# Kernel tuning notes

Measured on AMD Instinct MI355X. Metric: run time of the kernel, lower is better.

Reference implementation:

```python
import jax, jax.numpy as jnp
import numpy as np

NEG_SLOPE = 0.2  # PyG GATConv default negative_slope


def gat_conv(x, edge_index, W, att_src, att_dst, bias):
    """PyG-style GATConv (concat heads, add_self_loops=True, eval mode).
    x: [N, F_in], edge_index: [2, E] (row 0 = src j, row 1 = dst i).
    W: [F_in, H*C], att_src/att_dst: [H, C], bias: [H*C].
    """
    N = x.shape[0]
    H, C = att_src.shape
    loops = jnp.arange(N, dtype=edge_index.dtype)
    src = jnp.concatenate([edge_index[0], loops])  # [E+N]
    dst = jnp.concatenate([edge_index[1], loops])
    h = (x @ W).reshape(N, H, C)                              # [N,H,C]
    a_src = jnp.einsum('nhc,hc->nh', h, att_src)              # [N,H]
    a_dst = jnp.einsum('nhc,hc->nh', h, att_dst)
    alpha = jax.nn.leaky_relu(a_src[src] + a_dst[dst], NEG_SLOPE)  # [E+N,H]
    # segment softmax over edges sharing the same destination node
    m = jax.ops.segment_max(alpha, dst, num_segments=N)       # [N,H]
    e = jnp.exp(alpha - jax.lax.stop_gradient(m)[dst])
    denom = jax.ops.segment_sum(e, dst, num_segments=N)       # [N,H]
    a = e / (denom[dst] + 1e-16)                              # [E+N,H]
    msg = h[src] * a[:, :, None]                              # [E+N,H,C]
    out = jax.ops.segment_sum(msg, dst, num_segments=N)       # [N,H,C]
    return out.reshape(N, H * C) + bias


def setup_inputs() -> dict:
    key = jax.random.key(0)
    ks = jax.random.split(key, 10)
    N, F, NC, C1, H1 = 50000, 128, 40, 16, 8
    E = 800000
    x = jax.random.normal(ks[0], (N, F), dtype=jnp.float32)
    edge_index = jax.random.randint(ks[1], (2, E), 0, N, dtype=jnp.int64)
    s1 = 1.0 / np.sqrt(F)
    W1 = jax.random.uniform(ks[2], (F, H1 * C1), jnp.float32, -s1, s1)
    att_src1 = jax.random.uniform(ks[3], (H1, C1), jnp.float32, -1.0, 1.0) * s1
    att_dst1 = jax.random.uniform(ks[4], (H1, C1), jnp.float32, -1.0, 1.0) * s1
    bias1 = jnp.zeros((H1 * C1,), jnp.float32)
    s2 = 1.0 / np.sqrt(H1 * C1)
    W2 = jax.random.uniform(ks[5], (H1 * C1, NC), jnp.float32, -s2, s2)
    att_src2 = jax.random.uniform(ks[6], (1, NC), jnp.float32, -1.0, 1.0) * s2
    att_dst2 = jax.random.uniform(ks[7], (1, NC), jnp.float32, -1.0, 1.0) * s2
    bias2 = jnp.zeros((NC,), jnp.float32)
    return {"x": x, "edge_index": edge_index, "W1": W1, "att_src1": att_src1,
            "att_dst1": att_dst1, "bias1": bias1, "W2": W2, "att_src2": att_src2,
            "att_dst2": att_dst2, "bias2": bias2}


def reference(x, edge_index, W1, att_src1, att_dst1, bias1, W2, att_src2, att_dst2, bias2):
    h = gat_conv(x, edge_index, W1, att_src1, att_dst1, bias1)   # [N, 128]
    # dropout in eval mode = identity
    out = gat_conv(h, edge_index, W2, att_src2, att_dst2, bias2)  # [N, 40]
    return out
```

## Files before the change

### kernel.cpp

```cpp
#include <hip/hip_runtime.h>
#include <hip/hip_bf16.h>
#include <math.h>

#define NEG_SLOPE 0.2f

__device__ __forceinline__ float lrelu(float x) { return x > 0.f ? x : NEG_SLOPE * x; }

__device__ __forceinline__ unsigned int pack_bf2(float a, float b) {
    unsigned int ua = __float_as_uint(a);
    ua = (ua + 0x7fffu + ((ua >> 16) & 1u)) >> 16;
    unsigned int ub = __float_as_uint(b);
    ub = (ub + 0x7fffu + ((ub >> 16) & 1u)) & 0xffff0000u;
    return ua | ub;
}
__device__ __forceinline__ float bf_lo(unsigned int u) { return __uint_as_float(u << 16); }
__device__ __forceinline__ float bf_hi(unsigned int u) { return __uint_as_float(u & 0xffff0000u); }

__global__ __launch_bounds__(256) void k_hist(const int* __restrict__ ei, int E, int N,
                                              int* __restrict__ cnt, int* __restrict__ rank) {
    int e = blockIdx.x * 256 + threadIdx.x;
    if (e >= E + N) return;
    int d = (e < E) ? ei[E + e] : (e - E);
    rank[e] = atomicAdd(&cnt[d], 1);
}

__global__ __launch_bounds__(256) void k_scan_part(const int* __restrict__ cnt, int N,
                                                   int* __restrict__ psum) {
    __shared__ int sh[256];
    int t = threadIdx.x;
    int base = blockIdx.x * 1024 + t * 4;
    int tl = 0;
#pragma unroll
    for (int j = 0; j < 4; ++j) tl += (base + j < N) ? cnt[base + j] : 0;
    sh[t] = tl; __syncthreads();
    for (int off = 128; off > 0; off >>= 1) {
        if (t < off) sh[t] += sh[t + off];
        __syncthreads();
    }
    if (t == 0) psum[blockIdx.x] = sh[0];
}

__global__ __launch_bounds__(256) void k_scan_mid(int* __restrict__ psum, int nb) {
    __shared__ int sh[256];
    int t = threadIdx.x;
    int v = (t < nb) ? psum[t] : 0;
    sh[t] = v; __syncthreads();
    for (int off = 1; off < 256; off <<= 1) {
        int a = (t >= off) ? sh[t - off] : 0;
        __syncthreads();
        sh[t] += a;
        __syncthreads();
    }
    psum[t] = sh[t] - v;
}

__global__ __launch_bounds__(256) void k_scan_add(const int* __restrict__ cnt, int N,
                                                  const int* __restrict__ psum,
                                                  int* __restrict__ rowptr) {
    __shared__ int sh[256];
    int t = threadIdx.x;
    int base = blockIdx.x * 1024 + t * 4;
    int c[4]; int tl = 0;
#pragma unroll
    for (int j = 0; j < 4; ++j) { c[j] = (base + j < N) ? cnt[base + j] : 0; tl += c[j]; }
    sh[t] = tl; __syncthreads();
    for (int off = 1; off < 256; off <<= 1) {
        int a = (t >= off) ? sh[t - off] : 0;
        __syncthreads();
        sh[t] += a;
        __syncthreads();
    }
    int run = psum[blockIdx.x] + (sh[t] - tl);
#pragma unroll
    for (int j = 0; j < 4; ++j) {
        if (base + j < N) { rowptr[base + j] = run; run += c[j]; }
    }
}

__global__ __launch_bounds__(256) void k_scatter(const int* __restrict__ ei, int E, int N,
                                                 const int* __restrict__ rowptr,
                                                 const int* __restrict__ rank,
                                                 int* __restrict__ col) {
    int e = blockIdx.x * 256 + threadIdx.x;
    if (e >= E + N) return;
    int s, d;
    if (e < E) { s = ei[e]; d = ei[E + e]; } else { s = d = e - E; }
    col[rowptr[d] + rank[e]] = s;
}

__global__ __launch_bounds__(256) void k_gemm1(const float* __restrict__ x,
                                               const float* __restrict__ W,
                                               const float* __restrict__ att_s,
                                               const float* __restrict__ att_d,
                                               unsigned int* __restrict__ h1A,
                                               unsigned int* __restrict__ h1B,
                                               float* __restrict__ a_src,
                                               float* __restrict__ a_dst, int N) {
    __shared__ float Wc[64 * 128];
    int t = threadIdx.x;
    int rg = t >> 4;
    int cg = t & 15;
    int row0 = blockIdx.x * 64 + rg * 4;
    int col0 = cg * 8;

    const float* xr[4];
#pragma unroll
    for (int j = 0; j < 4; ++j) {
        int r = row0 + j; r = (r < N) ? r : (N - 1);
        xr[j] = x + (size_t)r * 128;
    }

    float acc[4][8];
#pragma unroll
    for (int j = 0; j < 4; ++j)
#pragma unroll
        for (int c = 0; c < 8; ++c) acc[j][c] = 0.f;

    for (int kc = 0; kc < 2; ++kc) {
        __syncthreads();
#pragma unroll
        for (int i = 0; i < 8; ++i) {
            int off = t * 4 + i * 1024;
            *(float4*)&Wc[off] = *(const float4*)&W[kc * 64 * 128 + off];
        }
        __syncthreads();

        for (int k0 = 0; k0 < 64; k0 += 4) {
            int kg = kc * 64 + k0;
            float4 xv[4];
#pragma unroll
            for (int j = 0; j < 4; ++j) xv[j] = *(const float4*)&xr[j][kg];
#pragma unroll
            for (int jj = 0; jj < 4; ++jj) {
                float4 w0 = *(const float4*)&Wc[(k0 + jj) * 128 + col0];
                float4 w1 = *(const float4*)&Wc[(k0 + jj) * 128 + col0 + 4];
#pragma unroll
                for (int j = 0; j < 4; ++j) {
                    float xs = (&xv[j].x)[jj];
                    acc[j][0] = fmaf(xs, w0.x, acc[j][0]);
                    acc[j][1] = fmaf(xs, w0.y, acc[j][1]);
                    acc[j][2] = fmaf(xs, w0.z, acc[j][2]);
                    acc[j][3] = fmaf(xs, w0.w, acc[j][3]);
                    acc[j][4] = fmaf(xs, w1.x, acc[j][4]);
                    acc[j][5] = fmaf(xs, w1.y, acc[j][5]);
                    acc[j][6] = fmaf(xs, w1.z, acc[j][6]);
                    acc[j][7] = fmaf(xs, w1.w, acc[j][7]);
                }
            }
        }
    }

    float as8[8], ad8[8];
#pragma unroll
    for (int c = 0; c < 8; ++c) { as8[c] = att_s[col0 + c]; ad8[c] = att_d[col0 + c]; }
    unsigned int* hp = (cg < 8) ? h1A : h1B;
    int loff = (cg & 7) * 4;
#pragma unroll
    for (int j = 0; j < 4; ++j) {
        int g = row0 + j;
        float ps = 0.f, pd = 0.f;
#pragma unroll
        for (int c = 0; c < 8; ++c) {
            ps = fmaf(acc[j][c], as8[c], ps);
            pd = fmaf(acc[j][c], ad8[c], pd);
        }
        ps += __shfl_xor(ps, 1);
        pd += __shfl_xor(pd, 1);
        if (g < N) {
            uint4 p = make_uint4(pack_bf2(acc[j][0], acc[j][1]), pack_bf2(acc[j][2], acc[j][3]),
                                 pack_bf2(acc[j][4], acc[j][5]), pack_bf2(acc[j][6], acc[j][7]));
            *(uint4*)&hp[(size_t)g * 32 + loff] = p;
            if ((t & 1) == 0) {
                int head = cg >> 1;
                a_src[(size_t)g * 8 + head] = ps;
                a_dst[(size_t)g * 8 + head] = pd;
            }
        }
    }
}

__global__ __launch_bounds__(256) void k_aggr1(const int* __restrict__ rowptr,
                                               const int* __restrict__ cnt,
                                               const int* __restrict__ col,
                                               const float* __restrict__ a_src,
                                               const float* __restrict__ a_dst,
                                               const unsigned int* __restrict__ hp,
                                               const float* __restrict__ bias1,
                                               float* __restrict__ out1, int N, int p) {
    __shared__ float evs[4][2][128];
    __shared__ int   cls[4][2][32];
    int t = threadIdx.x;
    int w = t >> 6;
    int lane = t & 63;
    int half = lane >> 5;
    int u = lane & 31;
    int node = blockIdx.x * 8 + w * 2 + half;
    bool nv = (node < N);
    int nodec = nv ? node : (N - 1);
    int beg = rowptr[nodec];
    int deg = nv ? cnt[nodec] : 0;
    int degO = __shfl_xor(deg, 32);
    int degmax = (deg > degO) ? deg : degO;
    if (degmax <= 0) return;

    int hh = u >> 3;
    float adh = a_dst[(size_t)nodec * 8 + p * 4 + hh];
    float4 ad4 = *(const float4*)&a_dst[(size_t)nodec * 8 + p * 4];

    float* myev = &evs[w][half][0];
    int*   mycl = &cls[w][half][0];

    float den = 0.f, n0 = 0.f, n1 = 0.f;
    int c = 0;
    while (c < degmax) {
        int slot = c + u;
        int slotc = (slot < deg) ? slot : (deg - 1);
        if (slotc < 0) slotc = 0;
        int su = col[beg + slotc];
        float4 as4 = *(const float4*)&a_src[(size_t)su * 8 + p * 4];
        bool valid = (slot < deg);
        float e0 = valid ? __expf(lrelu(as4.x + ad4.x)) : 0.f;
        float e1 = valid ? __expf(lrelu(as4.y + ad4.y)) : 0.f;
        float e2 = valid ? __expf(lrelu(as4.z + ad4.z)) : 0.f;
        float e3 = valid ? __expf(lrelu(as4.w + ad4.w)) : 0.f;
        *(float4*)&myev[u * 4] = make_float4(e0, e1, e2, e3);
        mycl[u] = su;

        int ccm = degmax - c; ccm = (ccm < 32) ? ccm : 32;
        int sP = mycl[0];
        unsigned int uP = hp[sP * 32 + u];
        for (int i = 0; i < ccm; ++i) {
            int in = (i + 1 < ccm) ? (i + 1) : i;
            int sN = mycl[in];
            unsigned int uN = hp[sN * 32 + u];
            float ev = myev[i * 4 + hh];
            den += ev;
            n0 = fmaf(ev, bf_lo(uP), n0);
            n1 = fmaf(ev, bf_hi(uP), n1);
            uP = uN;
        }
        c += 32;
    }
    if (nv) {
        float inv = 1.f / (den + 1e-16f);
        int ch = p * 64 + 2 * u;
        float2 b = *(const float2*)&bias1[ch];
        float2 o = make_float2(fmaf(n0, inv, b.x), fmaf(n1, inv, b.y));
        *(float2*)&out1[(size_t)node * 128 + ch] = o;
    }
}

__global__ __launch_bounds__(256) void k_gemm2(const float* __restrict__ out1,
                                               const float* __restrict__ W2,
                                               const float* __restrict__ att_s2,
                                               const float* __restrict__ att_d2,
                                               unsigned int* __restrict__ h2b,
                                               float* __restrict__ a_src2,
                                               float* __restrict__ a_dst2, int N) {
    __shared__ float Ws[128 * 40];
    int t = threadIdx.x;
    for (int i = t * 4; i < 128 * 40; i += 256 * 4)
        *(float4*)&Ws[i] = *(const float4*)&W2[i];
    __syncthreads();
    int n = blockIdx.x * 256 + t;
    if (n >= N) return;

    float acc[40];
#pragma unroll
    for (int c = 0; c < 40; ++c) acc[c] = 0.f;

    for (int k0 = 0; k0 < 128; k0 += 4) {
        float4 v = *(const float4*)&out1[(size_t)n * 128 + k0];
        float xj[4] = {v.x, v.y, v.z, v.w};
#pragma unroll
        for (int j = 0; j < 4; ++j) {
            float xb = xj[j];
#pragma unroll
            for (int c0 = 0; c0 < 40; c0 += 4) {
                float4 w = *(const float4*)&Ws[(k0 + j) * 40 + c0];
                acc[c0 + 0] = fmaf(xb, w.x, acc[c0 + 0]);
                acc[c0 + 1] = fmaf(xb, w.y, acc[c0 + 1]);
                acc[c0 + 2] = fmaf(xb, w.z, acc[c0 + 2]);
                acc[c0 + 3] = fmaf(xb, w.w, acc[c0 + 3]);
            }
        }
    }
    float s2 = 0.f, d2 = 0.f;
#pragma unroll
    for (int c = 0; c < 40; ++c) {
        s2 = fmaf(acc[c], att_s2[c], s2);
        d2 = fmaf(acc[c], att_d2[c], d2);
    }
    unsigned int p[20];
#pragma unroll
    for (int j = 0; j < 20; ++j) p[j] = pack_bf2(acc[2 * j], acc[2 * j + 1]);
#pragma unroll
    for (int j = 0; j < 5; ++j)
        *(uint4*)&h2b[(size_t)n * 20 + 4 * j] = make_uint4(p[4 * j], p[4 * j + 1], p[4 * j + 2], p[4 * j + 3]);
    a_src2[n] = s2;
    a_dst2[n] = d2;
}

__global__ __launch_bounds__(256) void k_aggr2(const int* __restrict__ rowptr,
                                               const int* __restrict__ cnt,
                                               const int* __restrict__ col,
                                               const float* __restrict__ a_src,
                                               const float* __restrict__ a_dst,
                                               const unsigned int* __restrict__ h2b,
                                               const float* __restrict__ bias2,
                                               float* __restrict__ out, int N) {
    __shared__ float evs[4][2][32];
    __shared__ int   cls[4][2][32];
    int t = threadIdx.x;
    int w = t >> 6;
    int lane = t & 63;
    int half = lane >> 5;
    int u = lane & 31;
    int node = blockIdx.x * 8 + w * 2 + half;
    bool nv = (node < N);
    int nodec = nv ? node : (N - 1);
    int beg = rowptr[nodec];
    int deg = nv ? cnt[nodec] : 0;
    int degO = __shfl_xor(deg, 32);
    int degmax = (deg > degO) ? deg : degO;
    if (degmax <= 0) return;

    int ucl = (u < 20) ? u : 19;
    float ad = a_dst[nodec];
    float* myev = &evs[w][half][0];
    int*   mycl = &cls[w][half][0];

    float den = 0.f, a0 = 0.f, a1 = 0.f;
    int c = 0;
    while (c < degmax) {
        int slot = c + u;
        int slotc = (slot < deg) ? slot : (deg - 1);
        if (slotc < 0) slotc = 0;
        int su = col[beg + slotc];
        float ev = (slot < deg) ? __expf(lrelu(a_src[su] + ad)) : 0.f;
        myev[u] = ev;
        mycl[u] = su;

        int ccm = degmax - c; ccm = (ccm < 32) ? ccm : 32;
        int sP = mycl[0];
        unsigned int uP = h2b[sP * 20 + ucl];
        for (int i = 0; i < ccm; ++i) {
            int in = (i + 1 < ccm) ? (i + 1) : i;
            int sN = mycl[in];
            unsigned int uN = h2b[sN * 20 + ucl];
            float evv = myev[i];
            den += evv;
            a0 = fmaf(evv, bf_lo(uP), a0);
            a1 = fmaf(evv, bf_hi(uP), a1);
            uP = uN;
        }
        c += 32;
    }
    if (nv && u < 20) {
        float inv = 1.f / (den + 1e-16f);
        float2 b = *(const float2*)&bias2[2 * u];
        float2 o = make_float2(fmaf(a0, inv, b.x), fmaf(a1, inv, b.y));
        *(float2*)&out[(size_t)node * 40 + 2 * u] = o;
    }
}

extern "C" void kernel_launch(void* const* d_in, const int* in_sizes, int n_in,
                              void* d_out, int out_size, void* d_ws, size_t ws_size,
                              hipStream_t stream) {
    const float* x   = (const float*)d_in[0];
    const int*   ei  = (const int*)d_in[1];
    const float* W1  = (const float*)d_in[2];
    const float* as1 = (const float*)d_in[3];
    const float* ad1 = (const float*)d_in[4];
    const float* b1  = (const float*)d_in[5];
    const float* W2  = (const float*)d_in[6];
    const float* as2 = (const float*)d_in[7];
    const float* ad2 = (const float*)d_in[8];
    const float* b2  = (const float*)d_in[9];

    int N = in_sizes[0] / 128;
    int E = in_sizes[1] / 2;
    int EN = E + N;
    size_t Np = (size_t)((N + 3) & ~3);
    size_t ENp = ((size_t)EN + 3) & ~3;

    float* ws = (float*)d_ws;
    float* out1    = ws; ws += Np * 128;
    unsigned int* h1A = (unsigned int*)ws; ws += Np * 32;
    unsigned int* h1Bp = (unsigned int*)ws; ws += Np * 32;
    unsigned int* h2b = (unsigned int*)ws; ws += Np * 20;
    float* a_src1  = ws; ws += Np * 8;
    float* a_dst1  = ws; ws += Np * 8;
    float* a_src2v = ws; ws += Np;
    float* a_dst2v = ws; ws += Np;
    int* cnt    = (int*)ws; ws += Np;
    int* rowptr = (int*)ws; ws += Np;
    int* psum   = (int*)ws; ws += 256;
    int* col    = (int*)ws; ws += ENp;
    int* rank   = (int*)ws; ws += ENp;

    int nb = (N + 1023) / 1024;

    hipMemsetAsync(cnt, 0, (size_t)N * sizeof(int), stream);
    k_hist<<<(EN + 255) / 256, 256, 0, stream>>>(ei, E, N, cnt, rank);
    k_scan_part<<<nb, 256, 0, stream>>>(cnt, N, psum);
    k_scan_mid<<<1, 256, 0, stream>>>(psum, nb);
    k_scan_add<<<nb, 256, 0, stream>>>(cnt, N, psum, rowptr);
    k_scatter<<<(EN + 255) / 256, 256, 0, stream>>>(ei, E, N, rowptr, rank, col);

    k_gemm1<<<(N + 63) / 64, 256, 0, stream>>>(x, W1, as1, ad1, h1A, h1Bp, a_src1, a_dst1, N);
    int nag = (N + 7) / 8;
    k_aggr1<<<nag, 256, 0, stream>>>(rowptr, cnt, col, a_src1, a_dst1, h1A, b1, out1, N, 0);
    k_aggr1<<<nag, 256, 0, stream>>>(rowptr, cnt, col, a_src1, a_dst1, h1Bp, b1, out1, N, 1);
    k_gemm2<<<(N + 255) / 256, 256, 0, stream>>>(out1, W2, as2, ad2, h2b, a_src2v, a_dst2v, N);
    k_aggr2<<<nag, 256, 0, stream>>>(rowptr, cnt, col, a_src2v, a_dst2v, h2b, b2, (float*)d_out, N);
}
```

Baseline: 274.0 us.

## Compute layer-1 GEMM with bf16 MFMA using split-precision x and prepacked W

```diff
diff --git a/kernel.cpp b/kernel.cpp
--- a/kernel.cpp
+++ b/kernel.cpp
@@ -3,6 +3,9 @@
 #include <math.h>
 
 #define NEG_SLOPE 0.2f
+
+typedef __bf16 bf16x8 __attribute__((ext_vector_type(8)));
+typedef float f32x4 __attribute__((ext_vector_type(4)));
 
 __device__ __forceinline__ float lrelu(float x) { return x > 0.f ? x : NEG_SLOPE * x; }
 
@@ -12,6 +15,10 @@
     unsigned int ub = __float_as_uint(b);
     ub = (ub + 0x7fffu + ((ub >> 16) & 1u)) & 0xffff0000u;
     return ua | ub;
+}
+__device__ __forceinline__ unsigned short f2bfu(float f) {
+    unsigned int ua = __float_as_uint(f);
+    return (unsigned short)((ua + 0x7fffu + ((ua >> 16) & 1u)) >> 16);
 }
 __device__ __forceinline__ float bf_lo(unsigned int u) { return __uint_as_float(u << 16); }
 __device__ __forceinline__ float bf_hi(unsigned int u) { return __uint_as_float(u & 0xffff0000u); }
@@ -88,92 +95,90 @@
     col[rowptr[d] + rank[e]] = s;
 }
 
+__global__ __launch_bounds__(256) void k_wpack(const float* __restrict__ W,
+                                               bf16x8* __restrict__ Wp) {
+    int idx = blockIdx.x * 256 + threadIdx.x;
+    if (idx >= 2048) return;
+    int n = idx & 15, quad = (idx >> 4) & 3, c = (idx >> 6) & 3, ct = idx >> 8;
+    bf16x8 v;
+#pragma unroll
+    for (int j = 0; j < 8; ++j)
+        v[j] = (__bf16)W[(c * 32 + quad * 8 + j) * 128 + ct * 16 + n];
+    Wp[idx] = v;
+}
+
 __global__ __launch_bounds__(256) void k_gemm1(const float* __restrict__ x,
-                                               const float* __restrict__ W,
+                                               const bf16x8* __restrict__ Wp,
                                                const float* __restrict__ att_s,
                                                const float* __restrict__ att_d,
-                                               unsigned int* __restrict__ h1A,
-                                               unsigned int* __restrict__ h1B,
+                                               unsigned short* __restrict__ h1A,
+                                               unsigned short* __restrict__ h1B,
                                                float* __restrict__ a_src,
                                                float* __restrict__ a_dst, int N) {
-    __shared__ float Wc[64 * 128];
-    int t = threadIdx.x;
-    int rg = t >> 4;
-    int cg = t & 15;
-    int row0 = blockIdx.x * 64 + rg * 4;
-    int col0 = cg * 8;
-
-    const float* xr[4];
-#pragma unroll
-    for (int j = 0; j < 4; ++j) {
-        int r = row0 + j; r = (r < N) ? r : (N - 1);
-        xr[j] = x + (size_t)r * 128;
-    }
-
-    float acc[4][8];
-#pragma unroll
-    for (int j = 0; j < 4; ++j)
-#pragma unroll
-        for (int c = 0; c < 8; ++c) acc[j][c] = 0.f;
-
-    for (int kc = 0; kc < 2; ++kc) {
-        __syncthreads();
-#pragma unroll
-        for (int i = 0; i < 8; ++i) {
-            int off = t * 4 + i * 1024;
-            *(float4*)&Wc[off] = *(const float4*)&W[kc * 64 * 128 + off];
-        }
-        __syncthreads();
-
-        for (int k0 = 0; k0 < 64; k0 += 4) {
-            int kg = kc * 64 + k0;
-            float4 xv[4];
-#pragma unroll
-            for (int j = 0; j < 4; ++j) xv[j] = *(const float4*)&xr[j][kg];
-#pragma unroll
-            for (int jj = 0; jj < 4; ++jj) {
-                float4 w0 = *(const float4*)&Wc[(k0 + jj) * 128 + col0];
-                float4 w1 = *(const float4*)&Wc[(k0 + jj) * 128 + col0 + 4];
-#pragma unroll
-                for (int j = 0; j < 4; ++j) {
-                    float xs = (&xv[j].x)[jj];
-                    acc[j][0] = fmaf(xs, w0.x, acc[j][0]);
-                    acc[j][1] = fmaf(xs, w0.y, acc[j][1]);
-                    acc[j][2] = fmaf(xs, w0.z, acc[j][2]);
-                    acc[j][3] = fmaf(xs, w0.w, acc[j][3]);
-                    acc[j][4] = fmaf(xs, w1.x, acc[j][4]);
-                    acc[j][5] = fmaf(xs, w1.y, acc[j][5]);
-                    acc[j][6] = fmaf(xs, w1.z, acc[j][6]);
-                    acc[j][7] = fmaf(xs, w1.w, acc[j][7]);
+    int t = threadIdx.x;
+    int w = t >> 6, lane = t & 63, quad = lane >> 4, n16 = lane & 15;
+    int row0 = blockIdx.x * 64 + w * 16;
+    int arow = row0 + n16; if (arow >= N) arow = N - 1;
+    const float* px = x + (size_t)arow * 128;
+
+    bf16x8 ah[4], al[4];
+#pragma unroll
+    for (int c = 0; c < 4; ++c) {
+        float4 v0 = *(const float4*)&px[c * 32 + quad * 8];
+        float4 v1 = *(const float4*)&px[c * 32 + quad * 8 + 4];
+        float xf[8] = {v0.x, v0.y, v0.z, v0.w, v1.x, v1.y, v1.z, v1.w};
+#pragma unroll
+        for (int j = 0; j < 8; ++j) {
+            __bf16 hi = (__bf16)xf[j];
+            ah[c][j] = hi;
+            al[c][j] = (__bf16)(xf[j] - (float)hi);
+        }
+    }
+
+    f32x4 acc[8];
+#pragma unroll
+    for (int ct = 0; ct < 8; ++ct) acc[ct] = (f32x4){0.f, 0.f, 0.f, 0.f};
+
+    const uint4* wp4 = (const uint4*)Wp;
+#pragma unroll
+    for (int ct = 0; ct < 8; ++ct) {
+#pragma unroll
+        for (int c = 0; c < 4; ++c) {
+            union { uint4 u; bf16x8 b; } bu;
+            bu.u = wp4[((ct * 4 + c) * 4 + quad) * 16 + n16];
+            acc[ct] = __builtin_amdgcn_mfma_f32_16x16x32_bf16(ah[c], bu.b, acc[ct], 0, 0, 0);
+            acc[ct] = __builtin_amdgcn_mfma_f32_16x16x32_bf16(al[c], bu.b, acc[ct], 0, 0, 0);
+        }
+    }
+
+    float asv[8], adv[8];
+#pragma unroll
+    for (int ct = 0; ct < 8; ++ct) {
+        asv[ct] = att_s[ct * 16 + n16];
+        adv[ct] = att_d[ct * 16 + n16];
+    }
+    int nodeb = row0 + quad * 4;
+#pragma unroll
+    for (int ct = 0; ct < 8; ++ct) {
+        unsigned short* hp = (ct < 4) ? h1A : h1B;
+        int chl = (ct & 3) * 16 + n16;
+#pragma unroll
+        for (int reg = 0; reg < 4; ++reg) {
+            int node = nodeb + reg;
+            float hv = acc[ct][reg];
+            float ps = hv * asv[ct];
+            float pd = hv * adv[ct];
+#pragma unroll
+            for (int m = 1; m < 16; m <<= 1) {
+                ps += __shfl_xor(ps, m);
+                pd += __shfl_xor(pd, m);
+            }
+            if (node < N) {
+                hp[(size_t)node * 64 + chl] = f2bfu(hv);
+                if (n16 == 0) {
+                    a_src[(size_t)node * 8 + ct] = ps;
+                    a_dst[(size_t)node * 8 + ct] = pd;
                 }
-            }
-        }
-    }
-
-    float as8[8], ad8[8];
-#pragma unroll
-    for (int c = 0; c < 8; ++c) { as8[c] = att_s[col0 + c]; ad8[c] = att_d[col0 + c]; }
-    unsigned int* hp = (cg < 8) ? h1A : h1B;
-    int loff = (cg & 7) * 4;
-#pragma unroll
-    for (int j = 0; j < 4; ++j) {
-        int g = row0 + j;
-        float ps = 0.f, pd = 0.f;
-#pragma unroll
-        for (int c = 0; c < 8; ++c) {
-            ps = fmaf(acc[j][c], as8[c], ps);
-            pd = fmaf(acc[j][c], ad8[c], pd);
-        }
-        ps += __shfl_xor(ps, 1);
-        pd += __shfl_xor(pd, 1);
-        if (g < N) {
-            uint4 p = make_uint4(pack_bf2(acc[j][0], acc[j][1]), pack_bf2(acc[j][2], acc[j][3]),
-                                 pack_bf2(acc[j][4], acc[j][5]), pack_bf2(acc[j][6], acc[j][7]));
-            *(uint4*)&hp[(size_t)g * 32 + loff] = p;
-            if ((t & 1) == 0) {
-                int head = cg >> 1;
-                a_src[(size_t)g * 8 + head] = ps;
-                a_dst[(size_t)g * 8 + head] = pd;
             }
         }
     }
@@ -204,7 +209,6 @@
     if (degmax <= 0) return;
 
     int hh = u >> 3;
-    float adh = a_dst[(size_t)nodec * 8 + p * 4 + hh];
     float4 ad4 = *(const float4*)&a_dst[(size_t)nodec * 8 + p * 4];
 
     float* myev = &evs[w][half][0];
@@ -277,11 +281,11 @@
             float xb = xj[j];
 #pragma unroll
             for (int c0 = 0; c0 < 40; c0 += 4) {
-                float4 w = *(const float4*)&Ws[(k0 + j) * 40 + c0];
-                acc[c0 + 0] = fmaf(xb, w.x, acc[c0 + 0]);
-                acc[c0 + 1] = fmaf(xb, w.y, acc[c0 + 1]);
-                acc[c0 + 2] = fmaf(xb, w.z, acc[c0 + 2]);
-                acc[c0 + 3] = fmaf(xb, w.w, acc[c0 + 3]);
+                float4 wv = *(const float4*)&Ws[(k0 + j) * 40 + c0];
+                acc[c0 + 0] = fmaf(xb, wv.x, acc[c0 + 0]);
+                acc[c0 + 1] = fmaf(xb, wv.y, acc[c0 + 1]);
+                acc[c0 + 2] = fmaf(xb, wv.z, acc[c0 + 2]);
+                acc[c0 + 3] = fmaf(xb, wv.w, acc[c0 + 3]);
             }
         }
     }
@@ -393,6 +397,7 @@
     float* a_dst1  = ws; ws += Np * 8;
     float* a_src2v = ws; ws += Np;
     float* a_dst2v = ws; ws += Np;
+    bf16x8* Wp = (bf16x8*)ws; ws += 2048 * 4;
     int* cnt    = (int*)ws; ws += Np;
     int* rowptr = (int*)ws; ws += Np;
     int* psum   = (int*)ws; ws += 256;
@@ -402,13 +407,16 @@
     int nb = (N + 1023) / 1024;
 
     hipMemsetAsync(cnt, 0, (size_t)N * sizeof(int), stream);
+    k_wpack<<<8, 256, 0, stream>>>(W1, Wp);
     k_hist<<<(EN + 255) / 256, 256, 0, stream>>>(ei, E, N, cnt, rank);
     k_scan_part<<<nb, 256, 0, stream>>>(cnt, N, psum);
     k_scan_mid<<<1, 256, 0, stream>>>(psum, nb);
     k_scan_add<<<nb, 256, 0, stream>>>(cnt, N, psum, rowptr);
     k_scatter<<<(EN + 255) / 256, 256, 0, stream>>>(ei, E, N, rowptr, rank, col);
 
-    k_gemm1<<<(N + 63) / 64, 256, 0, stream>>>(x, W1, as1, ad1, h1A, h1Bp, a_src1, a_dst1, N);
+    k_gemm1<<<(N + 63) / 64, 256, 0, stream>>>(x, Wp, as1, ad1,
+                                               (unsigned short*)h1A, (unsigned short*)h1Bp,
+                                               a_src1, a_dst1, N);
     int nag = (N + 7) / 8;
     k_aggr1<<<nag, 256, 0, stream>>>(rowptr, cnt, col, a_src1, a_dst1, h1A, b1, out1, N, 0);
     k_aggr1<<<nag, 256, 0, stream>>>(rowptr, cnt, col, a_src1, a_dst1, h1Bp, b1, out1, N, 1);
```

Result: faster. 266.1 us (-2.9%).
